# Kernel optimization log

Hardware: AMD Instinct MI355X
Metric: run time of the kernel (lower is better)

## Reference

```python
import jax, jax.numpy as jnp
import numpy as np

D_MODEL = 1024
N_HEADS = 16
HEAD_DIM = D_MODEL // N_HEADS
WINDOW = 128
ROPE_BASE = 10000.0


def _rope_cos_sin(T, dim, dtype):
    inv_freq = 1.0 / (ROPE_BASE ** (jnp.arange(0, dim, 2, dtype=jnp.float32) / dim))
    freqs = jnp.arange(T, dtype=jnp.float32)[:, None] * inv_freq[None, :]  # [T, dim/2]
    emb = jnp.concatenate([freqs, freqs], axis=-1)  # [T, dim]
    return jnp.cos(emb).astype(dtype), jnp.sin(emb).astype(dtype)


def _rotate_half(x):
    h = x.shape[-1] // 2
    return jnp.concatenate([-x[..., h:], x[..., :h]], axis=-1)


def _apply_rotary(x, cos, sin):
    # x: [B, T, H, Dh]; cos/sin: [T, Dh]
    c = cos[None, :, None, :]
    s = sin[None, :, None, :]
    return x * c + _rotate_half(x) * s


def setup_inputs() -> dict:
    key = jax.random.key(0)
    ks = jax.random.split(key, 6)
    B, T = 2, 2048
    query = jax.random.normal(ks[0], (B, T, D_MODEL), dtype=jnp.float32)
    scale = 1.0 / np.sqrt(D_MODEL)
    Wq = jax.random.normal(ks[1], (D_MODEL, D_MODEL), dtype=jnp.float32) * scale
    Wk = jax.random.normal(ks[2], (D_MODEL, D_MODEL), dtype=jnp.float32) * scale
    Wv = jax.random.normal(ks[3], (D_MODEL, D_MODEL), dtype=jnp.float32) * scale
    Wo = jax.random.normal(ks[4], (D_MODEL, D_MODEL), dtype=jnp.float32) * scale
    bo = jax.random.normal(ks[5], (D_MODEL,), dtype=jnp.float32) * 0.01
    return {"query": query, "Wq": Wq, "Wk": Wk, "Wv": Wv, "Wo": Wo, "bo": bo}


def reference(query, Wq, Wk, Wv, Wo, bo):
    # Sliding-window causal self-attention with rotary embeddings (eval mode, no dropout).
    B, T, D = query.shape
    H, Dh = N_HEADS, HEAD_DIM
    sm_scale = Dh ** -0.5

    # Projections (torch nn.Linear: y = x @ W.T)
    q = (query @ Wq.T).reshape(B, T, H, Dh)
    k = (query @ Wk.T).reshape(B, T, H, Dh)
    v = (query @ Wv.T).reshape(B, T, H, Dh)

    cos, sin = _rope_cos_sin(T, Dh, query.dtype)
    q = _apply_rotary(q, cos, sin)
    k = _apply_rotary(k, cos, sin)

    # [B, H, T, Dh]
    q = q.transpose(0, 2, 1, 3)
    k = k.transpose(0, 2, 1, 3)
    v = v.transpose(0, 2, 1, 3)

    scores = jnp.einsum('bhqd,bhkd->bhqk', q, k) * sm_scale

    # Causal sliding-window mask: masked if j > i or j < i - (WINDOW - 1)
    i = jnp.arange(T)[:, None]
    j = jnp.arange(T)[None, :]
    mask = (j > i) | (j < i - (WINDOW - 1))  # [T, T], True = masked
    scores = jnp.where(mask[None, None], jnp.float32(-jnp.inf), scores)

    attn = jax.nn.softmax(scores, axis=-1)
    out = jnp.einsum('bhqk,bhkd->bhqd', attn, v)  # [B, H, T, Dh]
    out = out.transpose(0, 2, 1, 3).reshape(B, T, D)
    return out @ Wo.T + bo
```

## Files before the change

### kernel.cpp

```cpp
#include <hip/hip_runtime.h>

#define BATCH 2
#define SEQ   2048
#define DMODEL 1024
#define NHEADS 16
#define HDIM   64
#define WINDOW 128
#define ROWS  (BATCH * SEQ)

typedef __bf16 bf16x8 __attribute__((ext_vector_type(8)));
typedef __bf16 bf16x4 __attribute__((ext_vector_type(4)));
typedef float  f32x4  __attribute__((ext_vector_type(4)));

__device__ __forceinline__ void async_load16(const __bf16* g, __bf16* l) {
    __builtin_amdgcn_global_load_lds(
        (const __attribute__((address_space(1))) unsigned int*)g,
        (__attribute__((address_space(3))) unsigned int*)l, 16, 0, 0);
}

__global__ __launch_bounds__(256) void convert_bf16(
    const float* __restrict__ X,
    const float* __restrict__ Wq, const float* __restrict__ Wk,
    const float* __restrict__ Wv, const float* __restrict__ Wo,
    __bf16* __restrict__ Xbf, __bf16* __restrict__ Wbf,
    float* __restrict__ ct, float* __restrict__ st)
{
    const int XN = ROWS * DMODEL / 4;
    const int WN = DMODEL * DMODEL / 4;
    const int TOT = XN + 4 * WN;
    int idx = blockIdx.x * blockDim.x + threadIdx.x;

    if (idx < TOT) {
        const float* src;
        __bf16* dst;
        if (idx < XN) {
            src = X + (size_t)idx * 4;
            dst = Xbf + (size_t)idx * 4;
        } else {
            int rel = idx - XN;
            int w = rel / WN;
            int off = rel - w * WN;
            const float* Wp = (w == 0) ? Wq : (w == 1) ? Wk : (w == 2) ? Wv : Wo;
            src = Wp + (size_t)off * 4;
            dst = Wbf + (size_t)rel * 4;
        }
        float4 v = *(const float4*)src;
        bf16x4 o;
        o[0] = (__bf16)v.x; o[1] = (__bf16)v.y; o[2] = (__bf16)v.z; o[3] = (__bf16)v.w;
        *(bf16x4*)dst = o;
    } else if (idx < TOT + SEQ * 32) {
        int k = idx - TOT;
        int t = k >> 5, d = k & 31;
        float ang = (float)t * expf(-(float)d * 0.28782313662425572f);
        float s, c;
        sincosf(ang, &s, &c);
        ct[k] = c; st[k] = s;
    }
}

template<int TM, int TN>
__device__ __forceinline__ void gemm_mfma_body(
    const __bf16* __restrict__ A, const __bf16* __restrict__ B,
    void* __restrict__ Cout, const float* __restrict__ bias,
    const float* __restrict__ ct, const float* __restrict__ st,
    int mode, int N, int K, int m0, int n0)
{
    constexpr bool SQ = (TN == 128);
    constexpr int NI = SQ ? 4 : (TM / 64);
    constexpr int NAC = TM / 64;
    constexpr int NBC = TN / 64;
    __shared__ __bf16 As[4][TM * 32];
    __shared__ __bf16 Bs[4][TN * 32];

    const int tid  = threadIdx.x;
    const int lane = tid & 63;
    const int wv   = tid >> 6;
    const int wrow = SQ ? (wv >> 1) * 64 : wv * (TM / 4);
    const int wcol = SQ ? (wv & 1) * 64 : 0;

    const int srow = lane >> 2;
    const int schk = (lane & 3) ^ ((lane >> 3) & 3);
    const int arbase = wv * (TM / 4);
    const int brbase = wv * (TN / 4);

    const __bf16* gA0 = A + (size_t)(m0 + arbase + srow) * K + 8 * schk;
    const __bf16* gA1 = gA0 + (size_t)16 * K;
    const __bf16* gB0 = B + (size_t)(n0 + brbase + srow) * K + 8 * schk;
    const __bf16* gB1 = gB0 + (size_t)16 * K;

    const int frow = lane & 15;
    const int fsw  = 8 * ((lane >> 4) ^ ((frow >> 1) & 3));

    f32x4 acc[NI][4];
#pragma unroll
    for (int i = 0; i < NI; ++i)
#pragma unroll
        for (int j = 0; j < 4; ++j) {
            acc[i][j][0] = 0.f; acc[i][j][1] = 0.f;
            acc[i][j][2] = 0.f; acc[i][j][3] = 0.f;
        }

    for (int k0 = 0; k0 < K; k0 += 128) {
        __syncthreads();
#pragma unroll
        for (int h = 0; h < 4; ++h) {
            async_load16(gA0 + k0 + 32 * h, As[h] + arbase * 32);
            if (NAC == 2)
                async_load16(gA1 + k0 + 32 * h, As[h] + (arbase + 16) * 32);
            async_load16(gB0 + k0 + 32 * h, Bs[h] + brbase * 32);
            if (NBC == 2)
                async_load16(gB1 + k0 + 32 * h, Bs[h] + (brbase + 16) * 32);
        }
        __syncthreads();

#pragma unroll
        for (int h = 0; h < 4; ++h) {
            bf16x8 afr[NI], bfr[4];
#pragma unroll
            for (int i = 0; i < NI; ++i)
                afr[i] = *(const bf16x8*)(As[h] + (wrow + 16 * i + frow) * 32 + fsw);
#pragma unroll
            for (int j = 0; j < 4; ++j)
                bfr[j] = *(const bf16x8*)(Bs[h] + (wcol + 16 * j + frow) * 32 + fsw);
#pragma unroll
            for (int i = 0; i < NI; ++i)
#pragma unroll
                for (int j = 0; j < 4; ++j)
                    acc[i][j] = __builtin_amdgcn_mfma_f32_16x16x32_bf16(
                        afr[i], bfr[j], acc[i][j], 0, 0, 0);
        }
    }

#pragma unroll
    for (int i = 0; i < NI; ++i) {
#pragma unroll
        for (int r = 0; r < 4; ++r) {
            int row = m0 + wrow + i * 16 + (lane >> 4) * 4 + r;
            if (mode <= 1) {
                int t = row & (SEQ - 1);
#pragma unroll
                for (int j = 0; j < 2; ++j) {
                    int dd = j * 16 + (lane & 15);
                    float c = ct[t * 32 + dd];
                    float s = st[t * 32 + dd];
                    float v0 = acc[i][j][r], v1 = acc[i][j + 2][r];
                    float n0v = v0 * c - v1 * s;
                    float n1v = v1 * c + v0 * s;
                    if (mode == 0) { n0v *= 0.125f; n1v *= 0.125f; }
                    acc[i][j][r] = n0v; acc[i][j + 2][r] = n1v;
                }
            }
#pragma unroll
            for (int j = 0; j < 4; ++j) {
                int col = n0 + wcol + j * 16 + (lane & 15);
                float v = acc[i][j][r];
                if (mode == 3)
                    ((float*)Cout)[(size_t)row * N + col] = v + bias[col];
                else
                    ((__bf16*)Cout)[(size_t)row * N + col] = (__bf16)v;
            }
        }
    }
}

template<int GX, int GY>
__device__ __forceinline__ void xcd_swizzle(int& xb, int& yb)
{
    int id = blockIdx.x + GX * blockIdx.y;
    int q  = id & 7;
    int s  = id >> 3;
    xb = s % GX;
    yb = (GY / 8) * q + s / GX;
}

__global__ __launch_bounds__(256) void gemm_qkv_bf(
    const __bf16* __restrict__ X, const __bf16* __restrict__ Wbf,
    __bf16* __restrict__ Qb, __bf16* __restrict__ Kb, __bf16* __restrict__ Vb,
    const float* __restrict__ ct, const float* __restrict__ st)
{
    const int z = blockIdx.z;
    const __bf16* W = Wbf + (size_t)z * (DMODEL * DMODEL);
    __bf16* C = (z == 0) ? Qb : (z == 1) ? Kb : Vb;
    int xb, yb;
    xcd_swizzle<8, 32>(xb, yb);
    gemm_mfma_body<128, 128>(X, W, C, nullptr, ct, st, z, DMODEL, DMODEL,
                             yb * 128, xb * 128);
}

__global__ __launch_bounds__(256) void gemm_out_bf(
    const __bf16* __restrict__ Abf, const __bf16* __restrict__ Wo,
    const float* __restrict__ bias, float* __restrict__ out)
{
    int xb, yb;
    xcd_swizzle<16, 64>(xb, yb);
    gemm_mfma_body<64, 64>(Abf, Wo, out, bias, nullptr, nullptr, 3,
                           DMODEL, DMODEL, yb * 64, xb * 64);
}

#define QTILE 64
#define KPAD  72
#define VPAD  216
#define PPAD  168

__global__ __launch_bounds__(256) void attn_mfma(
    const __bf16* __restrict__ Qb, const __bf16* __restrict__ Kb,
    const __bf16* __restrict__ Vb, __bf16* __restrict__ Abf)
{
    __shared__ __bf16 KsPs[192 * KPAD];
    __shared__ __bf16 Vt[64 * VPAD];

    const int tid  = threadIdx.x;
    const int lane = tid & 63;
    const int wv   = tid >> 6;
    const int q0   = blockIdx.x * QTILE;
    const int h    = blockIdx.y;
    const int b    = blockIdx.z;
    const int jbase = q0 - 128;
    const size_t hoff = (size_t)h * HDIM;
    const int nloc  = lane & 15;
    const int mbase = (lane >> 4) * 4;
    const int fk    = (lane >> 4) * 8;

    const __bf16* Kg = Kb + (size_t)(b * SEQ) * DMODEL + hoff;
    const __bf16* Vg = Vb + (size_t)(b * SEQ) * DMODEL + hoff;

#pragma unroll
    for (int it = 0; it < 6; ++it) {
        int idx = tid + it * 256;
        int jt = idx >> 3;
        int dq = (idx & 7) * 8;
        int jg = jbase + jt;
        int jc = jg < 0 ? 0 : jg;
        bf16x8 kv = *(const bf16x8*)(Kg + (size_t)jc * DMODEL + dq);
        bf16x8 vv = *(const bf16x8*)(Vg + (size_t)jc * DMODEL + dq);
        *(bf16x8*)(KsPs + jt * KPAD + dq) = kv;
#pragma unroll
        for (int e = 0; e < 8; ++e) Vt[(dq + e) * VPAD + jt] = vv[e];
    }
#pragma unroll
    for (int it = 0; it < 4; ++it) {
        int idx = tid + it * 256;
        int d = idx >> 4, c = idx & 15;
        Vt[d * VPAD + 192 + c] = (__bf16)0.0f;
    }
    __syncthreads();

    const __bf16* Qg = Qb + (size_t)(b * SEQ + q0 + 16 * wv + nloc) * DMODEL + hoff + fk;
    bf16x8 qfr0 = *(const bf16x8*)(Qg);
    bf16x8 qfr1 = *(const bf16x8*)(Qg + 32);

    f32x4 s[9];
#pragma unroll
    for (int c = 0; c < 9; ++c) {
        const __bf16* kp = KsPs + (size_t)(16 * (wv + c) + nloc) * KPAD + fk;
        bf16x8 k0 = *(const bf16x8*)kp;
        bf16x8 k1 = *(const bf16x8*)(kp + 32);
        f32x4 z; z[0] = 0.f; z[1] = 0.f; z[2] = 0.f; z[3] = 0.f;
        z = __builtin_amdgcn_mfma_f32_16x16x32_bf16(qfr0, k0, z, 0, 0, 0);
        z = __builtin_amdgcn_mfma_f32_16x16x32_bf16(qfr1, k1, z, 0, 0, 0);
        s[c] = z;
    }
    __syncthreads();

    float inv_row[4];
#pragma unroll
    for (int r = 0; r < 4; ++r) {
        int rl = 16 * wv + mbase + r;
        float mx = -INFINITY;
#pragma unroll
        for (int c = 0; c < 9; ++c) {
            int jt = 16 * (wv + c) + nloc;
            bool valid = (jt >= rl + 1) && (jt <= rl + 128) && (jbase + jt >= 0);
            float sv = valid ? s[c][r] : -INFINITY;
            s[c][r] = sv;
            mx = fmaxf(mx, sv);
        }
#pragma unroll
        for (int off = 8; off; off >>= 1) mx = fmaxf(mx, __shfl_xor(mx, off));
        float sum = 0.f;
#pragma unroll
        for (int c = 0; c < 9; ++c) {
            float p = __expf(s[c][r] - mx);
            s[c][r] = p;
            sum += p;
        }
#pragma unroll
        for (int off = 8; off; off >>= 1) sum += __shfl_xor(sum, off);
        inv_row[r] = 1.0f / sum;
    }

    __bf16* myP = KsPs + (size_t)wv * 16 * PPAD;
#pragma unroll
    for (int c = 0; c < 9; ++c)
#pragma unroll
        for (int r = 0; r < 4; ++r)
            myP[(mbase + r) * PPAD + 16 * c + nloc] = (__bf16)(s[c][r] * inv_row[r]);
#pragma unroll
    for (int r = 0; r < 4; ++r)
        myP[(mbase + r) * PPAD + 144 + nloc] = (__bf16)0.0f;

    asm volatile("" ::: "memory");
    __builtin_amdgcn_s_waitcnt(0);

    f32x4 o[4];
#pragma unroll
    for (int j = 0; j < 4; ++j) { o[j][0] = 0.f; o[j][1] = 0.f; o[j][2] = 0.f; o[j][3] = 0.f; }
#pragma unroll
    for (int stp = 0; stp < 5; ++stp) {
        bf16x8 pf = *(const bf16x8*)(myP + nloc * PPAD + 32 * stp + fk);
#pragma unroll
        for (int j = 0; j < 4; ++j) {
            bf16x8 vf = *(const bf16x8*)(Vt + (size_t)(16 * j + nloc) * VPAD
                                         + 16 * wv + 32 * stp + fk);
            o[j] = __builtin_amdgcn_mfma_f32_16x16x32_bf16(pf, vf, o[j], 0, 0, 0);
        }
    }

    __bf16* Og = Abf + (size_t)(b * SEQ + q0 + 16 * wv) * DMODEL + hoff;
#pragma unroll
    for (int j = 0; j < 4; ++j)
#pragma unroll
        for (int r = 0; r < 4; ++r)
            Og[(size_t)(mbase + r) * DMODEL + 16 * j + nloc] = (__bf16)o[j][r];
}

extern "C" void kernel_launch(void* const* d_in, const int* in_sizes, int n_in,
                              void* d_out, int out_size, void* d_ws, size_t ws_size,
                              hipStream_t stream)
{
    const float* X  = (const float*)d_in[0];
    const float* Wq = (const float*)d_in[1];
    const float* Wk = (const float*)d_in[2];
    const float* Wv = (const float*)d_in[3];
    const float* Wo = (const float*)d_in[4];
    const float* bo = (const float*)d_in[5];
    float* out = (float*)d_out;

    const size_t MB = 1ull << 20;
    __bf16* Xbf = (__bf16*)d_ws;
    __bf16* Wbf = (__bf16*)((char*)d_ws + 8 * MB);
    __bf16* Qb  = (__bf16*)((char*)d_ws + 16 * MB);
    __bf16* Kb  = (__bf16*)((char*)d_ws + 24 * MB);
    __bf16* Vb  = (__bf16*)((char*)d_ws + 32 * MB);
    float*  ctab = (float*)((char*)d_ws + 40 * MB);
    float*  stab = (float*)((char*)d_ws + 41 * MB);
    __bf16* Abf = Xbf;

    {
        int total = (ROWS * DMODEL + 4 * DMODEL * DMODEL) / 4 + SEQ * 32;
        convert_bf16<<<(total + 255) / 256, 256, 0, stream>>>(
            X, Wq, Wk, Wv, Wo, Xbf, Wbf, ctab, stab);
    }
    {
        dim3 grid(DMODEL / 128, ROWS / 128, 3);
        gemm_qkv_bf<<<grid, 256, 0, stream>>>(Xbf, Wbf, Qb, Kb, Vb, ctab, stab);
    }
    {
        dim3 grid(SEQ / QTILE, NHEADS, BATCH);
        attn_mfma<<<grid, 256, 0, stream>>>(Qb, Kb, Vb, Abf);
    }
    {
        dim3 grid(DMODEL / 64, ROWS / 64, 1);
        gemm_out_bf<<<grid, 256, 0, stream>>>(Abf, Wbf + 3ull * DMODEL * DMODEL, bo, out);
    }
}
```

Before: 165.3 us.

## Replace QKV GEMM with 256x256-tile 8-wave kernel using phased MFMA schedule

```diff
diff --git a/kernel.cpp b/kernel.cpp
--- a/kernel.cpp
+++ b/kernel.cpp
@@ -58,6 +58,153 @@
     }
 }
 
+#define RAW_BAR __builtin_amdgcn_s_barrier()
+#define LGKM0   asm volatile("s_waitcnt lgkmcnt(0)" ::: "memory")
+#define VM0     asm volatile("s_waitcnt vmcnt(0)" ::: "memory")
+#define CFENCE  asm volatile("" ::: "memory")
+#define MFMA16(a, b, c) __builtin_amdgcn_mfma_f32_16x16x32_bf16(a, b, c, 0, 0, 0)
+
+__global__ __launch_bounds__(512, 2) void gemm_qkv_8ph(
+    const __bf16* __restrict__ X, const __bf16* __restrict__ Wbf,
+    __bf16* __restrict__ Qb, __bf16* __restrict__ Kb, __bf16* __restrict__ Vb,
+    const float* __restrict__ ct, const float* __restrict__ st)
+{
+    __shared__ __bf16 As[2][256 * 64];
+    __shared__ __bf16 Bs[2][256 * 64];
+
+    const int tid  = threadIdx.x;
+    const int lane = tid & 63;
+    const int wv   = tid >> 6;
+    const int wr   = wv >> 2;
+    const int wc   = wv & 3;
+
+    int id = blockIdx.x + 12 * blockIdx.y;
+    int tt = (id & 7) * 24 + (id >> 3);
+    const int xb = tt % 12, yb = tt / 12;
+    const int m0 = yb * 256;
+    const int n0 = xb * 256;
+
+    const int srow = wv * 16 + (lane >> 3);
+    const int schk = 8 * ((lane & 7) ^ (lane >> 3));
+    const __bf16* gA = X   + (size_t)(m0 + srow) * DMODEL + schk;
+    const __bf16* gB = Wbf + (size_t)(n0 + srow) * DMODEL + schk;
+    const int lbase = wv * 16 * 64;
+
+#define STAGE_A(buf, k0) do {                                          \
+    async_load16(gA + (k0),                &As[buf][lbase]);           \
+    async_load16(gA + (k0) + 8 * DMODEL,   &As[buf][lbase + 8 * 64]);  \
+    async_load16(gA + (k0) + 128 * DMODEL, &As[buf][lbase + 128 * 64]);\
+    async_load16(gA + (k0) + 136 * DMODEL, &As[buf][lbase + 136 * 64]);} while (0)
+#define STAGE_B(buf, k0) do {                                          \
+    async_load16(gB + (k0),                &Bs[buf][lbase]);           \
+    async_load16(gB + (k0) + 8 * DMODEL,   &Bs[buf][lbase + 8 * 64]);  \
+    async_load16(gB + (k0) + 128 * DMODEL, &Bs[buf][lbase + 128 * 64]);\
+    async_load16(gB + (k0) + 136 * DMODEL, &Bs[buf][lbase + 136 * 64]);} while (0)
+
+    const int frow = lane & 15;
+    const int hi   = lane >> 4;
+    const int s0   = 8 * (hi ^ (frow & 7));
+    const int s1   = 8 * ((4 + hi) ^ (frow & 7));
+    const int aoff = (wr * 128 + frow) * 64;
+    const int boff = (wc * 64 + frow) * 64;
+
+    f32x4 acc[8][4];
+#pragma unroll
+    for (int i = 0; i < 8; ++i)
+#pragma unroll
+        for (int j = 0; j < 4; ++j) {
+            acc[i][j][0] = 0.f; acc[i][j][1] = 0.f;
+            acc[i][j][2] = 0.f; acc[i][j][3] = 0.f;
+        }
+
+#define PHASE(I2, STAGE_STMT, VM_STMT) do {                                  \
+    STAGE_STMT;                                                              \
+    bf16x8 aA = *(const bf16x8*)&Ac[aoff + (I2) * 1024 + s0];                \
+    bf16x8 aB = *(const bf16x8*)&Ac[aoff + (I2) * 1024 + s1];                \
+    bf16x8 aC = *(const bf16x8*)&Ac[aoff + (I2) * 1024 + 1024 + s0];         \
+    bf16x8 aD = *(const bf16x8*)&Ac[aoff + (I2) * 1024 + 1024 + s1];         \
+    CFENCE; RAW_BAR; CFENCE; LGKM0;                                          \
+    __builtin_amdgcn_s_setprio(1);                                           \
+    acc[I2][0] = MFMA16(aA, bfr[0][0], acc[I2][0]);                          \
+    acc[I2][1] = MFMA16(aA, bfr[1][0], acc[I2][1]);                          \
+    acc[I2][2] = MFMA16(aA, bfr[2][0], acc[I2][2]);                          \
+    acc[I2][3] = MFMA16(aA, bfr[3][0], acc[I2][3]);                          \
+    acc[I2][0] = MFMA16(aB, bfr[0][1], acc[I2][0]);                          \
+    acc[I2][1] = MFMA16(aB, bfr[1][1], acc[I2][1]);                          \
+    acc[I2][2] = MFMA16(aB, bfr[2][1], acc[I2][2]);                          \
+    acc[I2][3] = MFMA16(aB, bfr[3][1], acc[I2][3]);                          \
+    acc[(I2)+1][0] = MFMA16(aC, bfr[0][0], acc[(I2)+1][0]);                  \
+    acc[(I2)+1][1] = MFMA16(aC, bfr[1][0], acc[(I2)+1][1]);                  \
+    acc[(I2)+1][2] = MFMA16(aC, bfr[2][0], acc[(I2)+1][2]);                  \
+    acc[(I2)+1][3] = MFMA16(aC, bfr[3][0], acc[(I2)+1][3]);                  \
+    acc[(I2)+1][0] = MFMA16(aD, bfr[0][1], acc[(I2)+1][0]);                  \
+    acc[(I2)+1][1] = MFMA16(aD, bfr[1][1], acc[(I2)+1][1]);                  \
+    acc[(I2)+1][2] = MFMA16(aD, bfr[2][1], acc[(I2)+1][2]);                  \
+    acc[(I2)+1][3] = MFMA16(aD, bfr[3][1], acc[(I2)+1][3]);                  \
+    __builtin_amdgcn_s_setprio(0);                                           \
+    VM_STMT;                                                                 \
+    CFENCE; RAW_BAR; CFENCE; } while (0)
+
+    STAGE_A(0, 0);
+    STAGE_B(0, 0);
+    VM0;
+    __syncthreads();
+
+#pragma unroll 2
+    for (int t = 0; t < 16; ++t) {
+        const int cur = t & 1, nxt = cur ^ 1;
+        const int k0 = t * 64;
+        const bool pre = (t < 15);
+        const __bf16* Ac = &As[cur][0];
+        const __bf16* Bc = &Bs[cur][0];
+
+        bf16x8 bfr[4][2];
+        if (pre) STAGE_A(nxt, k0 + 64);
+#pragma unroll
+        for (int j = 0; j < 4; ++j) {
+            bfr[j][0] = *(const bf16x8*)&Bc[boff + j * 1024 + s0];
+            bfr[j][1] = *(const bf16x8*)&Bc[boff + j * 1024 + s1];
+        }
+        PHASE(0, (void)0, (void)0);
+        PHASE(2, if (pre) STAGE_B(nxt, k0 + 64), (void)0);
+        PHASE(4, (void)0, (void)0);
+        PHASE(6, (void)0, VM0);
+    }
+
+    const int z = n0 >> 10;
+    __bf16* Cz = (z == 0) ? Qb : (z == 1) ? Kb : Vb;
+    const int ncol = n0 & 1023;
+#pragma unroll
+    for (int i = 0; i < 8; ++i) {
+#pragma unroll
+        for (int r = 0; r < 4; ++r) {
+            int row  = m0 + wr * 128 + i * 16 + hi * 4 + r;
+            int tpos = row & (SEQ - 1);
+            if (z <= 1) {
+#pragma unroll
+                for (int j = 0; j < 2; ++j) {
+                    int dd = j * 16 + frow;
+                    float c = ct[tpos * 32 + dd];
+                    float s = st[tpos * 32 + dd];
+                    float v0 = acc[i][j][r], v1 = acc[i][j + 2][r];
+                    float n0v = v0 * c - v1 * s;
+                    float n1v = v1 * c + v0 * s;
+                    if (z == 0) { n0v *= 0.125f; n1v *= 0.125f; }
+                    acc[i][j][r] = n0v; acc[i][j + 2][r] = n1v;
+                }
+            }
+#pragma unroll
+            for (int j = 0; j < 4; ++j) {
+                int col = ncol + wc * 64 + j * 16 + frow;
+                Cz[(size_t)row * DMODEL + col] = (__bf16)acc[i][j][r];
+            }
+        }
+    }
+#undef PHASE
+#undef STAGE_A
+#undef STAGE_B
+}
+
 template<int TM, int TN>
 __device__ __forceinline__ void gemm_mfma_body(
     const __bf16* __restrict__ A, const __bf16* __restrict__ B,
@@ -173,20 +320,6 @@
     yb = (GY / 8) * q + s / GX;
 }
 
-__global__ __launch_bounds__(256) void gemm_qkv_bf(
-    const __bf16* __restrict__ X, const __bf16* __restrict__ Wbf,
-    __bf16* __restrict__ Qb, __bf16* __restrict__ Kb, __bf16* __restrict__ Vb,
-    const float* __restrict__ ct, const float* __restrict__ st)
-{
-    const int z = blockIdx.z;
-    const __bf16* W = Wbf + (size_t)z * (DMODEL * DMODEL);
-    __bf16* C = (z == 0) ? Qb : (z == 1) ? Kb : Vb;
-    int xb, yb;
-    xcd_swizzle<8, 32>(xb, yb);
-    gemm_mfma_body<128, 128>(X, W, C, nullptr, ct, st, z, DMODEL, DMODEL,
-                             yb * 128, xb * 128);
-}
-
 __global__ __launch_bounds__(256) void gemm_out_bf(
     const __bf16* __restrict__ Abf, const __bf16* __restrict__ Wo,
     const float* __restrict__ bias, float* __restrict__ out)
@@ -352,8 +485,8 @@
             X, Wq, Wk, Wv, Wo, Xbf, Wbf, ctab, stab);
     }
     {
-        dim3 grid(DMODEL / 128, ROWS / 128, 3);
-        gemm_qkv_bf<<<grid, 256, 0, stream>>>(Xbf, Wbf, Qb, Kb, Vb, ctab, stab);
+        dim3 grid(12, 16, 1);
+        gemm_qkv_8ph<<<grid, 512, 0, stream>>>(Xbf, Wbf, Qb, Kb, Vb, ctab, stab);
     }
     {
         dim3 grid(SEQ / QTILE, NHEADS, BATCH);
```

Result: no change. 164.6 us (-0.4%).

## Replace QKV GEMM with 256x256-tile 512-thread kernel using 4-stage async LDS ring

Applied to the files above, without the earlier changes.

```diff
diff --git a/kernel.cpp b/kernel.cpp
--- a/kernel.cpp
+++ b/kernel.cpp
@@ -58,6 +58,148 @@
     }
 }
 
+#define RAW_BAR __builtin_amdgcn_s_barrier()
+#define VM8     asm volatile("s_waitcnt vmcnt(8)" ::: "memory")
+#define VM4     asm volatile("s_waitcnt vmcnt(4)" ::: "memory")
+#define VM0     asm volatile("s_waitcnt vmcnt(0)" ::: "memory")
+#define CFENCE  asm volatile("" ::: "memory")
+#define MFMA16(a, b, c) __builtin_amdgcn_mfma_f32_16x16x32_bf16(a, b, c, 0, 0, 0)
+
+__global__ __launch_bounds__(512, 2) void gemm_qkv_ring(
+    const __bf16* __restrict__ X, const __bf16* __restrict__ Wbf,
+    __bf16* __restrict__ Qb, __bf16* __restrict__ Kb, __bf16* __restrict__ Vb,
+    const float* __restrict__ ct, const float* __restrict__ st)
+{
+    __shared__ __bf16 As[4 * 256 * 32];
+    __shared__ __bf16 Bs[4 * 256 * 32];
+
+    const int tid  = threadIdx.x;
+    const int lane = tid & 63;
+    const int wv   = tid >> 6;
+    const int wr   = wv >> 2;
+    const int wc   = wv & 3;
+
+    int id = blockIdx.x + 12 * blockIdx.y;
+    int tt = (id & 7) * 24 + (id >> 3);
+    const int xb = tt % 12, yb = tt / 12;
+    const int m0 = yb * 256;
+    const int n0 = xb * 256;
+
+    const int srow  = lane >> 2;
+    const int schk  = 8 * ((lane & 3) ^ ((lane >> 3) & 3));
+    const int abase = wv * 32;
+    const __bf16* gA = X   + (size_t)(m0 + abase + srow) * DMODEL + schk;
+    const __bf16* gB = Wbf + (size_t)(n0 + abase + srow) * DMODEL + schk;
+
+#define STAGE(RING, T) do {                                    \
+    __bf16* la = As + (RING) * 8192 + abase * 32;              \
+    __bf16* lb = Bs + (RING) * 8192 + abase * 32;              \
+    const int kk = (T) * 32;                                   \
+    async_load16(gA + kk,             la);                     \
+    async_load16(gA + kk + 16 * DMODEL, la + 512);             \
+    async_load16(gB + kk,             lb);                     \
+    async_load16(gB + kk + 16 * DMODEL, lb + 512);             \
+} while (0)
+
+    const int frow = lane & 15;
+    const int hi   = lane >> 4;
+    const int fsw  = 8 * (hi ^ ((frow >> 1) & 3));
+    const int aoff = (wr * 128 + frow) * 32 + fsw;
+    const int boff = (wc * 64 + frow) * 32 + fsw;
+
+    f32x4 acc[8][4];
+#pragma unroll
+    for (int i = 0; i < 8; ++i)
+#pragma unroll
+        for (int j = 0; j < 4; ++j) {
+            acc[i][j][0] = 0.f; acc[i][j][1] = 0.f;
+            acc[i][j][2] = 0.f; acc[i][j][3] = 0.f;
+        }
+
+#define ROW4(I, AF)                                                     \
+    acc[I][0] = MFMA16(AF, bfr0, acc[I][0]);                            \
+    acc[I][1] = MFMA16(AF, bfr1, acc[I][1]);                            \
+    acc[I][2] = MFMA16(AF, bfr2, acc[I][2]);                            \
+    acc[I][3] = MFMA16(AF, bfr3, acc[I][3]);
+
+#define ITER(RING, STAGE_STMT, VM_STMT) do {                            \
+    const __bf16* Asl = As + (RING) * 8192;                             \
+    const __bf16* Bsl = Bs + (RING) * 8192;                             \
+    STAGE_STMT;                                                         \
+    bf16x8 bfr0 = *(const bf16x8*)(Bsl + boff);                         \
+    bf16x8 bfr1 = *(const bf16x8*)(Bsl + boff + 512);                   \
+    bf16x8 bfr2 = *(const bf16x8*)(Bsl + boff + 1024);                  \
+    bf16x8 bfr3 = *(const bf16x8*)(Bsl + boff + 1536);                  \
+    bf16x8 af0 = *(const bf16x8*)(Asl + aoff);                          \
+    bf16x8 af1 = *(const bf16x8*)(Asl + aoff + 512);                    \
+    bf16x8 af2 = *(const bf16x8*)(Asl + aoff + 1024);                   \
+    bf16x8 af3 = *(const bf16x8*)(Asl + aoff + 1536);                   \
+    CFENCE; RAW_BAR; CFENCE;                                            \
+    __builtin_amdgcn_s_setprio(1);                                      \
+    ROW4(0, af0) ROW4(1, af1) ROW4(2, af2) ROW4(3, af3)                 \
+    __builtin_amdgcn_s_setprio(0);                                      \
+    CFENCE; RAW_BAR; CFENCE;                                            \
+    bf16x8 af4 = *(const bf16x8*)(Asl + aoff + 2048);                   \
+    bf16x8 af5 = *(const bf16x8*)(Asl + aoff + 2560);                   \
+    bf16x8 af6 = *(const bf16x8*)(Asl + aoff + 3072);                   \
+    bf16x8 af7 = *(const bf16x8*)(Asl + aoff + 3584);                   \
+    CFENCE; RAW_BAR; CFENCE;                                            \
+    __builtin_amdgcn_s_setprio(1);                                      \
+    ROW4(4, af4) ROW4(5, af5) ROW4(6, af6) ROW4(7, af7)                 \
+    __builtin_amdgcn_s_setprio(0);                                      \
+    VM_STMT;                                                            \
+    CFENCE; RAW_BAR; CFENCE;                                            \
+} while (0)
+
+    STAGE(0, 0); STAGE(1, 1); STAGE(2, 2);
+    VM8;
+    CFENCE; RAW_BAR; CFENCE;
+
+    for (int t = 0; t < 28; t += 4) {
+        ITER(0, STAGE(3, t + 3), VM8);
+        ITER(1, STAGE(0, t + 4), VM8);
+        ITER(2, STAGE(1, t + 5), VM8);
+        ITER(3, STAGE(2, t + 6), VM8);
+    }
+    ITER(0, STAGE(3, 31), VM8);
+    ITER(1, (void)0, VM4);
+    ITER(2, (void)0, VM0);
+    ITER(3, (void)0, (void)0);
+
+    const int z = n0 >> 10;
+    __bf16* Cz = (z == 0) ? Qb : (z == 1) ? Kb : Vb;
+    const int ncol = n0 & 1023;
+#pragma unroll
+    for (int i = 0; i < 8; ++i) {
+#pragma unroll
+        for (int r = 0; r < 4; ++r) {
+            int row  = m0 + wr * 128 + i * 16 + hi * 4 + r;
+            int tpos = row & (SEQ - 1);
+            if (z <= 1) {
+#pragma unroll
+                for (int j = 0; j < 2; ++j) {
+                    int dd = j * 16 + frow;
+                    float c = ct[tpos * 32 + dd];
+                    float s = st[tpos * 32 + dd];
+                    float v0 = acc[i][j][r], v1 = acc[i][j + 2][r];
+                    float n0v = v0 * c - v1 * s;
+                    float n1v = v1 * c + v0 * s;
+                    if (z == 0) { n0v *= 0.125f; n1v *= 0.125f; }
+                    acc[i][j][r] = n0v; acc[i][j + 2][r] = n1v;
+                }
+            }
+#pragma unroll
+            for (int j = 0; j < 4; ++j) {
+                int col = ncol + wc * 64 + j * 16 + frow;
+                Cz[(size_t)row * DMODEL + col] = (__bf16)acc[i][j][r];
+            }
+        }
+    }
+#undef ITER
+#undef ROW4
+#undef STAGE
+}
+
 template<int TM, int TN>
 __device__ __forceinline__ void gemm_mfma_body(
     const __bf16* __restrict__ A, const __bf16* __restrict__ B,
@@ -173,20 +315,6 @@
     yb = (GY / 8) * q + s / GX;
 }
 
-__global__ __launch_bounds__(256) void gemm_qkv_bf(
-    const __bf16* __restrict__ X, const __bf16* __restrict__ Wbf,
-    __bf16* __restrict__ Qb, __bf16* __restrict__ Kb, __bf16* __restrict__ Vb,
-    const float* __restrict__ ct, const float* __restrict__ st)
-{
-    const int z = blockIdx.z;
-    const __bf16* W = Wbf + (size_t)z * (DMODEL * DMODEL);
-    __bf16* C = (z == 0) ? Qb : (z == 1) ? Kb : Vb;
-    int xb, yb;
-    xcd_swizzle<8, 32>(xb, yb);
-    gemm_mfma_body<128, 128>(X, W, C, nullptr, ct, st, z, DMODEL, DMODEL,
-                             yb * 128, xb * 128);
-}
-
 __global__ __launch_bounds__(256) void gemm_out_bf(
     const __bf16* __restrict__ Abf, const __bf16* __restrict__ Wo,
     const float* __restrict__ bias, float* __restrict__ out)
@@ -352,8 +480,8 @@
             X, Wq, Wk, Wv, Wo, Xbf, Wbf, ctab, stab);
     }
     {
-        dim3 grid(DMODEL / 128, ROWS / 128, 3);
-        gemm_qkv_bf<<<grid, 256, 0, stream>>>(Xbf, Wbf, Qb, Kb, Vb, ctab, stab);
+        dim3 grid(12, 16, 1);
+        gemm_qkv_ring<<<grid, 512, 0, stream>>>(Xbf, Wbf, Qb, Kb, Vb, ctab, stab);
     }
     {
         dim3 grid(SEQ / QTILE, NHEADS, BATCH);
```

After: 169.0 us. +2.2%, slower.
